# Kernel tuning notes

Measured on AMD Instinct MI355X. Metric: run time of the kernel, lower is better.

The kernel has to match this reference:

```python
import jax, jax.numpy as jnp
import numpy as np

N_NODES = 50000
N_EDGES = 800000
ND = 64   # node_dim
HD = 128  # hidden_dim
ED = 32   # edge_dim


def setup_inputs() -> dict:
    key = jax.random.key(0)
    ks = jax.random.split(key, 16)
    init = lambda k, shape: (jax.random.normal(k, shape, jnp.float32)
                             / np.float32(np.sqrt(shape[0])))
    h = jax.random.normal(ks[0], (N_NODES, ND), jnp.float32)
    x = jax.random.normal(ks[1], (N_NODES, 3), jnp.float32) * 10.0
    edge_index = jax.random.randint(ks[2], (2, N_EDGES), 0, N_NODES, dtype=jnp.int64)
    # realistic edge distances = actual pairwise distances of sampled edges
    edge_dist = jnp.linalg.norm(x[edge_index[0]] - x[edge_index[1]], axis=-1)
    in_dim = 2 * ND + ED
    return {
        "h": h, "x": x, "edge_index": edge_index, "edge_dist": edge_dist,
        # edge_mlp: Linear(1, ED) -> SiLU -> Linear(ED, ED)
        "We1": init(ks[3], (1, ED)), "be1": jnp.zeros((ED,), jnp.float32),
        "We2": init(ks[4], (ED, ED)), "be2": jnp.zeros((ED,), jnp.float32),
        # node_mlp: Linear(in_dim, HD) -> SiLU -> Linear(HD, ND)
        "Wn1": init(ks[5], (in_dim, HD)), "bn1": jnp.zeros((HD,), jnp.float32),
        "Wn2": init(ks[6], (HD, ND)), "bn2": jnp.zeros((ND,), jnp.float32),
        # coord_mlp: Linear(in_dim, HD) -> SiLU -> Linear(HD, 1, bias=False)
        "Wc1": init(ks[7], (in_dim, HD)), "bc1": jnp.zeros((HD,), jnp.float32),
        "Wc2": init(ks[8], (HD, 1)),
    }


def reference(h, x, edge_index, edge_dist,
              We1, be1, We2, be2,
              Wn1, bn1, Wn2, bn2,
              Wc1, bc1, Wc2):
    n = h.shape[0]
    src, dst = edge_index[0], edge_index[1]
    # edge_mlp on scalar distance -> [E, ED]
    e = jax.nn.silu(edge_dist[:, None] @ We1 + be1) @ We2 + be2
    # gather + concat -> [E, 2*ND + ED]
    m_input = jnp.concatenate([h[src], h[dst], e], axis=-1)
    # node messages [E, ND]
    m = jax.nn.silu(m_input @ Wn1 + bn1) @ Wn2 + bn2
    h_agg = jax.ops.segment_sum(m, dst, num_segments=n)
    # coord update weight [E, 1]
    coord_weight = jax.nn.silu(m_input @ Wc1 + bc1) @ Wc2
    dir_vec = x[src] - x[dst]
    dir_len = jnp.clip(jnp.linalg.norm(dir_vec, axis=-1, keepdims=True), 1e-8)
    coord_update = coord_weight * (dir_vec / dir_len)
    x_agg = jax.ops.segment_sum(coord_update, dst, num_segments=n)
    return h + h_agg, x + x_agg
```

## Files before the change

kernel.cpp:

```cpp
#include <hip/hip_runtime.h>


#define NN 50000
#define NE 800000
#define NDIM 64
#define HDIM 128
#define EDIM 32
#define NTILES (NE / 64)
#define MSTRIDE 168
#define HSTRIDE 136
#define NH (NN * NDIM)
#define NX (NN * 3)

#define WS_WN1P 0
#define WS_WC1P 20480
#define WS_BN1P 40960
#define WS_BC1P 41088

typedef __bf16 bf16x8 __attribute__((ext_vector_type(8)));
typedef float f32x4 __attribute__((ext_vector_type(4)));
typedef unsigned short ushort8 __attribute__((ext_vector_type(8)));
typedef unsigned short ushort4v __attribute__((ext_vector_type(4)));

__device__ __forceinline__ unsigned short f2bf(float f) {
    union { __bf16 b; unsigned short u; } c;
    c.b = (__bf16)f;
    return c.u;
}
__device__ __forceinline__ float silu(float v) {
    return __fdividef(v, 1.0f + __expf(-v));
}

__device__ __forceinline__ void bar_lds() {
    asm volatile("s_waitcnt lgkmcnt(0)" ::: "memory");
    __builtin_amdgcn_s_barrier();
}

__device__ __forceinline__ bf16x8 ld_frag(const unsigned short* p) {
    union { ushort8 u; bf16x8 v; } c;
    c.u = *(const ushort8*)p;
    return c.v;
}
__device__ __forceinline__ bf16x8 mk_frag(const unsigned short* u) {
    union { ushort8 uu; bf16x8 v; } c;
#pragma unroll
    for (int j = 0; j < 8; ++j) c.uu[j] = u[j];
    return c.v;
}

__global__ void init_out(const float* __restrict__ h, const float* __restrict__ x,
                         float* __restrict__ out) {
    int i = blockIdx.x * 256 + threadIdx.x;
    if (i < NH) out[i] = h[i];
    else if (i < NH + NX) out[i] = x[i - NH];
}

__global__ __launch_bounds__(128) void fold_weights(
    const float* __restrict__ We2, const float* __restrict__ be2,
    const float* __restrict__ Wn1, const float* __restrict__ bn1,
    const float* __restrict__ Wc1, const float* __restrict__ bc1,
    float* __restrict__ ws) {
    const int b = blockIdx.x;
    const int col = threadIdx.x;
    if (b < 320) {
        const int path = (b >= 160);
        const float* W = path ? Wc1 : Wn1;
        float* Wp = ws + (path ? WS_WC1P : WS_WN1P);
        const int r = path ? (b - 160) : b;
        if (r < 128) {
            Wp[r * 128 + col] = W[r * 128 + col];
        } else {
            const int j = r - 128;
            float s = 0.0f;
#pragma unroll
            for (int n = 0; n < 32; ++n)
                s += We2[j * 32 + n] * W[(128 + n) * 128 + col];
            Wp[r * 128 + col] = s;
        }
    } else {
        const int path = b - 320;
        const float* W = path ? Wc1 : Wn1;
        const float* bb = path ? bc1 : bn1;
        float* bp = ws + (path ? WS_BC1P : WS_BN1P);
        float s = bb[col];
#pragma unroll
        for (int n = 0; n < 32; ++n)
            s += be2[n] * W[(128 + n) * 128 + col];
        bp[col] = s;
    }
}

__global__ __launch_bounds__(256, 2) void egnn_edges(
    const float* __restrict__ h, const float* __restrict__ x,
    const int* __restrict__ srcg, const int* __restrict__ dstg,
    const float* __restrict__ dist,
    const float* __restrict__ We1, const float* __restrict__ be1,
    const float* __restrict__ Wn2, const float* __restrict__ bn2,
    const float* __restrict__ Wc2,
    const float* __restrict__ wsW,
    float* __restrict__ outh, float* __restrict__ outx) {

    __shared__ __align__(16) unsigned short mlds[64 * MSTRIDE];
    __shared__ __align__(16) unsigned short hl[64 * HSTRIDE];
    __shared__ int src_l[64];
    __shared__ int dst_l[64];
    __shared__ float we1_l[32], be1_l[32];
    __shared__ float part_l[256];

    const int tid  = threadIdx.x;
    const int w    = tid >> 6;
    const int lane = tid & 63;
    const int l15  = lane & 15;
    const int quad = lane >> 4;

    const float* Wn1p = wsW + WS_WN1P;
    const float* Wc1p = wsW + WS_WC1P;
    const float* bn1p = wsW + WS_BN1P;
    const float* bc1p = wsW + WS_BC1P;

    if (tid < 32) { we1_l[tid] = We1[tid]; be1_l[tid] = be1[tid]; }

    bf16x8 wn1f[5][2], wc1f[5][2];
#pragma unroll
    for (int kc = 0; kc < 5; ++kc) {
#pragma unroll
        for (int nt = 0; nt < 2; ++nt) {
            unsigned short un[8], uc[8];
            const int n = w * 32 + nt * 16 + l15;
#pragma unroll
            for (int j = 0; j < 8; ++j) {
                const int k = kc * 32 + quad * 8 + j;
                un[j] = f2bf(Wn1p[k * HDIM + n]);
                uc[j] = f2bf(Wc1p[k * HDIM + n]);
            }
            wn1f[kc][nt] = mk_frag(un);
            wc1f[kc][nt] = mk_frag(uc);
        }
    }
    bf16x8 wn2f[4];
#pragma unroll
    for (int kc = 0; kc < 4; ++kc) {
        unsigned short u[8];
        const int n = w * 16 + l15;
#pragma unroll
        for (int j = 0; j < 8; ++j) {
            const int k = kc * 32 + quad * 8 + j;
            u[j] = f2bf(Wn2[k * NDIM + n]);
        }
        wn2f[kc] = mk_frag(u);
    }
    const float biasN0 = bn1p[w * 32 + l15];
    const float biasN1 = bn1p[w * 32 + 16 + l15];
    const float biasC0 = bc1p[w * 32 + l15];
    const float biasC1 = bc1p[w * 32 + 16 + l15];
    const float bias2v = bn2[w * 16 + l15];
    const float wcA = Wc2[w * 32 + l15];
    const float wcB = Wc2[w * 32 + 16 + l15];

    for (int tile = blockIdx.x; tile < NTILES; tile += gridDim.x) {
        int pf_s = 0, pf_d = 0;
        if (tid < 64) {
            const int e = tile * 64 + tid;
            pf_s = srcg[e];
            pf_d = dstg[e];
        }
        bar_lds();

        if (tid < 64) { src_l[tid] = pf_s; dst_l[tid] = pf_d; }
        bar_lds();

        {
            const int c4 = tid & 15, sub = tid >> 4;
#pragma unroll
            for (int it = 0; it < 4; ++it) {
                const int el = sub + it * 16;
                const float4 hs = *(const float4*)(h + (size_t)src_l[el] * NDIM + c4 * 4);
                const float4 hd = *(const float4*)(h + (size_t)dst_l[el] * NDIM + c4 * 4);
                ushort4v us = { f2bf(hs.x), f2bf(hs.y), f2bf(hs.z), f2bf(hs.w) };
                ushort4v ud = { f2bf(hd.x), f2bf(hd.y), f2bf(hd.z), f2bf(hd.w) };
                *(ushort4v*)&mlds[el * MSTRIDE + c4 * 4] = us;
                *(ushort4v*)&mlds[el * MSTRIDE + 64 + c4 * 4] = ud;
            }
        }
        {
            const int el = tid >> 2, j0 = (tid & 3) * 8;
            const float dv = dist[tile * 64 + el];
            ushort8 u;
#pragma unroll
            for (int j = 0; j < 8; ++j)
                u[j] = f2bf(silu(dv * we1_l[j0 + j] + be1_l[j0 + j]));
            *(ushort8*)&mlds[el * MSTRIDE + 128 + j0] = u;
        }
        bar_lds();

        f32x4 accN[4][2], accC[4][2];
#pragma unroll
        for (int mt = 0; mt < 4; ++mt) {
            accN[mt][0] = (f32x4){biasN0, biasN0, biasN0, biasN0};
            accN[mt][1] = (f32x4){biasN1, biasN1, biasN1, biasN1};
            accC[mt][0] = (f32x4){biasC0, biasC0, biasC0, biasC0};
            accC[mt][1] = (f32x4){biasC1, biasC1, biasC1, biasC1};
        }
#pragma unroll
        for (int kc = 0; kc < 5; ++kc) {
            bf16x8 af[4];
#pragma unroll
            for (int mt = 0; mt < 4; ++mt)
                af[mt] = ld_frag(&mlds[(mt * 16 + l15) * MSTRIDE + kc * 32 + quad * 8]);
#pragma unroll
            for (int mt = 0; mt < 4; ++mt) {
#pragma unroll
                for (int nt = 0; nt < 2; ++nt) {
                    accN[mt][nt] = __builtin_amdgcn_mfma_f32_16x16x32_bf16(
                        af[mt], wn1f[kc][nt], accN[mt][nt], 0, 0, 0);
                    accC[mt][nt] = __builtin_amdgcn_mfma_f32_16x16x32_bf16(
                        af[mt], wc1f[kc][nt], accC[mt][nt], 0, 0, 0);
                }
            }
        }

#pragma unroll
        for (int mt = 0; mt < 4; ++mt)
#pragma unroll
            for (int nt = 0; nt < 2; ++nt)
#pragma unroll
                for (int r = 0; r < 4; ++r)
                    hl[(mt * 16 + quad * 4 + r) * HSTRIDE + w * 32 + nt * 16 + l15] =
                        f2bf(silu(accN[mt][nt][r]));

        {
            float p[16];
#pragma unroll
            for (int mt = 0; mt < 4; ++mt)
#pragma unroll
                for (int r = 0; r < 4; ++r)
                    p[mt * 4 + r] = silu(accC[mt][0][r]) * wcA + silu(accC[mt][1][r]) * wcB;

            float q8[8];
#pragma unroll
            for (int i = 0; i < 8; ++i) {
                const float send = (l15 & 8) ? p[i] : p[i + 8];
                const float recv = __shfl_xor(send, 8, 64);
                q8[i] = ((l15 & 8) ? p[i + 8] : p[i]) + recv;
            }
            float q4[4];
#pragma unroll
            for (int i = 0; i < 4; ++i) {
                const float send = (l15 & 4) ? q8[i] : q8[i + 4];
                const float recv = __shfl_xor(send, 4, 64);
                q4[i] = ((l15 & 4) ? q8[i + 4] : q8[i]) + recv;
            }
            float q2[2];
#pragma unroll
            for (int i = 0; i < 2; ++i) {
                const float send = (l15 & 2) ? q4[i] : q4[i + 2];
                const float recv = __shfl_xor(send, 2, 64);
                q2[i] = ((l15 & 2) ? q4[i + 2] : q4[i]) + recv;
            }
            {
                const float send = (l15 & 1) ? q2[0] : q2[1];
                const float recv = __shfl_xor(send, 1, 64);
                const float tot = ((l15 & 1) ? q2[1] : q2[0]) + recv;
                const int edge = (l15 >> 2) * 16 + quad * 4 + (l15 & 3);
                part_l[w * 64 + edge] = tot;
            }
        }
        bar_lds();

        f32x4 acc2[4];
#pragma unroll
        for (int mt = 0; mt < 4; ++mt) acc2[mt] = (f32x4){bias2v, bias2v, bias2v, bias2v};
#pragma unroll
        for (int kc = 0; kc < 4; ++kc) {
#pragma unroll
            for (int mt = 0; mt < 4; ++mt) {
                bf16x8 a2 = ld_frag(&hl[(mt * 16 + l15) * HSTRIDE + kc * 32 + quad * 8]);
                acc2[mt] = __builtin_amdgcn_mfma_f32_16x16x32_bf16(a2, wn2f[kc], acc2[mt], 0, 0, 0);
            }
        }
#pragma unroll
        for (int mt = 0; mt < 4; ++mt) {
#pragma unroll
            for (int r = 0; r < 4; ++r) {
                const int el = mt * 16 + quad * 4 + r;
                atomicAdd(outh + (size_t)dst_l[el] * NDIM + w * 16 + l15, acc2[mt][r]);
            }
        }

        if (tid < 64) {
            const float cw = part_l[tid] + part_l[64 + tid] + part_l[128 + tid] + part_l[192 + tid];
            const int sn = src_l[tid], dn = dst_l[tid];
            const float dx = x[sn * 3 + 0] - x[dn * 3 + 0];
            const float dy = x[sn * 3 + 1] - x[dn * 3 + 1];
            const float dz = x[sn * 3 + 2] - x[dn * 3 + 2];
            float len = sqrtf(dx * dx + dy * dy + dz * dz);
            len = fmaxf(len, 1e-8f);
            const float f = cw / len;
            atomicAdd(outx + (size_t)dn * 3 + 0, f * dx);
            atomicAdd(outx + (size_t)dn * 3 + 1, f * dy);
            atomicAdd(outx + (size_t)dn * 3 + 2, f * dz);
        }
    }
}

extern "C" void kernel_launch(void* const* d_in, const int* in_sizes, int n_in,
                              void* d_out, int out_size, void* d_ws, size_t ws_size,
                              hipStream_t stream) {
    const float* h    = (const float*)d_in[0];
    const float* x    = (const float*)d_in[1];
    const int*   ei   = (const int*)d_in[2];
    const float* dist = (const float*)d_in[3];
    const float* We1  = (const float*)d_in[4];
    const float* be1  = (const float*)d_in[5];
    const float* We2  = (const float*)d_in[6];
    const float* be2  = (const float*)d_in[7];
    const float* Wn1  = (const float*)d_in[8];
    const float* bn1  = (const float*)d_in[9];
    const float* Wn2  = (const float*)d_in[10];
    const float* bn2  = (const float*)d_in[11];
    const float* Wc1  = (const float*)d_in[12];
    const float* bc1  = (const float*)d_in[13];
    const float* Wc2  = (const float*)d_in[14];

    float* outh = (float*)d_out;
    float* outx = outh + (size_t)NH;
    float* ws   = (float*)d_ws;

    fold_weights<<<322, 128, 0, stream>>>(We2, be2, Wn1, bn1, Wc1, bc1, ws);
    init_out<<<(NH + NX + 255) / 256, 256, 0, stream>>>(h, x, (float*)d_out);
    egnn_edges<<<1024, 256, 0, stream>>>(h, x, ei, ei + NE, dist,
                                         We1, be1, Wn2, bn2, Wc2, ws,
                                         outh, outx);
}
```

Measured before the change: 425.8 us.

## Sort edges by destination and pre-reduce messages before atomic scatter

Adds a counting sort of edges by destination node (histogram, three-pass scan, scatter into workspace) so the edge kernel processes edges grouped by dst. In the edge kernel, per-tile messages and coordinate updates are staged in LDS and run-length reduced over consecutive equal destinations before issuing atomics. This is meant to cut the number of global atomics (about 16 per node on average). The cost is six extra small kernels and extra global traffic for the sorted arrays, and the sort path only runs if the workspace is large enough.

```diff
diff --git a/kernel.cpp b/kernel.cpp
--- a/kernel.cpp
+++ b/kernel.cpp
@@ -9,6 +9,7 @@
 #define NTILES (NE / 64)
 #define MSTRIDE 168
 #define HSTRIDE 136
+#define MLSTRIDE 65
 #define NH (NN * NDIM)
 #define NX (NN * 3)
 
@@ -16,6 +17,15 @@
 #define WS_WC1P 20480
 #define WS_BN1P 40960
 #define WS_BC1P 41088
+#define WS_WEIGHTS_FLOATS 65536
+#define NCNT 50176
+#define IOFF_CNT    WS_WEIGHTS_FLOATS
+#define IOFF_BLK    (IOFF_CNT + NCNT)
+#define IOFF_CUR    (IOFF_BLK + 256)
+#define IOFF_SRCS   (IOFF_CUR + NCNT)
+#define IOFF_DSTS   (IOFF_SRCS + NE)
+#define IOFF_DISTS  (IOFF_DSTS + NE)
+#define WS_TOTAL_BYTES ((size_t)(IOFF_DISTS + NE) * 4)
 
 typedef __bf16 bf16x8 __attribute__((ext_vector_type(8)));
 typedef float f32x4 __attribute__((ext_vector_type(4)));
@@ -54,6 +64,71 @@
     if (i < NH) out[i] = h[i];
     else if (i < NH + NX) out[i] = x[i - NH];
 }
+
+
+__global__ __launch_bounds__(256) void zero_cnt(int* __restrict__ cnt, int* __restrict__ cur) {
+    const int i = blockIdx.x * 256 + threadIdx.x;
+    if (i < NCNT) { cnt[i] = 0; cur[i] = 0; }
+}
+
+__global__ __launch_bounds__(256) void hist_dst(const int* __restrict__ dst, int* __restrict__ cnt) {
+    const int e = blockIdx.x * 256 + threadIdx.x;
+    if (e < NE) atomicAdd(&cnt[dst[e]], 1);
+}
+
+__global__ __launch_bounds__(256) void scan1(int* __restrict__ cnt, int* __restrict__ blk) {
+    __shared__ int sh[256];
+    const int t = threadIdx.x, i = blockIdx.x * 256 + t;
+    const int v = cnt[i];
+    sh[t] = v;
+    __syncthreads();
+#pragma unroll
+    for (int d = 1; d < 256; d <<= 1) {
+        const int o = (t >= d) ? sh[t - d] : 0;
+        __syncthreads();
+        sh[t] += o;
+        __syncthreads();
+    }
+    cnt[i] = sh[t] - v;
+    if (t == 255) blk[blockIdx.x] = sh[t];
+}
+
+__global__ __launch_bounds__(256) void scan2(int* __restrict__ blk) {
+    __shared__ int sh[256];
+    const int t = threadIdx.x;
+    const int v = (t < 196) ? blk[t] : 0;
+    sh[t] = v;
+    __syncthreads();
+#pragma unroll
+    for (int d = 1; d < 256; d <<= 1) {
+        const int o = (t >= d) ? sh[t - d] : 0;
+        __syncthreads();
+        sh[t] += o;
+        __syncthreads();
+    }
+    if (t < 196) blk[t] = sh[t] - v;
+}
+
+__global__ __launch_bounds__(256) void scan3(int* __restrict__ cnt, const int* __restrict__ blk) {
+    const int i = blockIdx.x * 256 + threadIdx.x;
+    if (i < NCNT) cnt[i] += blk[blockIdx.x];
+}
+
+__global__ __launch_bounds__(256) void scatter_edges(
+    const int* __restrict__ src, const int* __restrict__ dst,
+    const float* __restrict__ dist,
+    const int* __restrict__ base, int* __restrict__ cur,
+    int* __restrict__ srcs, int* __restrict__ dsts, float* __restrict__ dists) {
+    const int e = blockIdx.x * 256 + threadIdx.x;
+    if (e < NE) {
+        const int d = dst[e];
+        const int pos = base[d] + atomicAdd(&cur[d], 1);
+        srcs[pos] = src[e];
+        dsts[pos] = d;
+        dists[pos] = dist[e];
+    }
+}
+
 
 __global__ __launch_bounds__(128) void fold_weights(
     const float* __restrict__ We2, const float* __restrict__ be2,
@@ -90,6 +165,7 @@
     }
 }
 
+
 __global__ __launch_bounds__(256, 2) void egnn_edges(
     const float* __restrict__ h, const float* __restrict__ x,
     const int* __restrict__ srcg, const int* __restrict__ dstg,
@@ -106,6 +182,7 @@
     __shared__ int dst_l[64];
     __shared__ float we1_l[32], be1_l[32];
     __shared__ float part_l[256];
+    __shared__ float cx_l[64], cy_l[64], cz_l[64];
 
     const int tid  = threadIdx.x;
     const int w    = tid >> 6;
@@ -278,13 +355,14 @@
                 acc2[mt] = __builtin_amdgcn_mfma_f32_16x16x32_bf16(a2, wn2f[kc], acc2[mt], 0, 0, 0);
             }
         }
-#pragma unroll
-        for (int mt = 0; mt < 4; ++mt) {
-#pragma unroll
-            for (int r = 0; r < 4; ++r) {
-                const int el = mt * 16 + quad * 4 + r;
-                atomicAdd(outh + (size_t)dst_l[el] * NDIM + w * 16 + l15, acc2[mt][r]);
-            }
+
+        {
+            float* ml = (float*)mlds;
+#pragma unroll
+            for (int mt = 0; mt < 4; ++mt)
+#pragma unroll
+                for (int r = 0; r < 4; ++r)
+                    ml[(mt * 16 + quad * 4 + r) * MLSTRIDE + w * 16 + l15] = acc2[mt][r];
         }
 
         if (tid < 64) {
@@ -296,9 +374,41 @@
             float len = sqrtf(dx * dx + dy * dy + dz * dz);
             len = fmaxf(len, 1e-8f);
             const float f = cw / len;
-            atomicAdd(outx + (size_t)dn * 3 + 0, f * dx);
-            atomicAdd(outx + (size_t)dn * 3 + 1, f * dy);
-            atomicAdd(outx + (size_t)dn * 3 + 2, f * dz);
+            cx_l[tid] = f * dx; cy_l[tid] = f * dy; cz_l[tid] = f * dz;
+        }
+        bar_lds();
+
+        {
+            const int c = lane, g = w;
+            const int r0 = g * 16;
+            float acc = ((const float*)mlds)[r0 * MLSTRIDE + c];
+            int d = dst_l[r0];
+#pragma unroll
+            for (int r = r0 + 1; r < r0 + 16; ++r) {
+                const int dn = dst_l[r];
+                if (dn != d) {
+                    atomicAdd(outh + (size_t)d * NDIM + c, acc);
+                    acc = 0.0f;
+                    d = dn;
+                }
+                acc += ((const float*)mlds)[r * MLSTRIDE + c];
+            }
+            atomicAdd(outh + (size_t)d * NDIM + c, acc);
+        }
+
+        if (tid < 64) {
+            const int d = dst_l[tid];
+            if (tid == 0 || dst_l[tid - 1] != d) {
+                float sx = 0.0f, sy = 0.0f, sz = 0.0f;
+                int r = tid;
+                do {
+                    sx += cx_l[r]; sy += cy_l[r]; sz += cz_l[r];
+                    ++r;
+                } while (r < 64 && dst_l[r] == d);
+                atomicAdd(outx + (size_t)d * 3 + 0, sx);
+                atomicAdd(outx + (size_t)d * 3 + 1, sy);
+                atomicAdd(outx + (size_t)d * 3 + 2, sz);
+            }
         }
     }
 }
@@ -328,7 +438,30 @@
 
     fold_weights<<<322, 128, 0, stream>>>(We2, be2, Wn1, bn1, Wc1, bc1, ws);
     init_out<<<(NH + NX + 255) / 256, 256, 0, stream>>>(h, x, (float*)d_out);
-    egnn_edges<<<1024, 256, 0, stream>>>(h, x, ei, ei + NE, dist,
+
+    const int* es = ei;
+    const int* ed = ei + NE;
+    const float* edist = dist;
+
+    if (ws_size >= WS_TOTAL_BYTES) {
+        int*   cnt   = (int*)d_ws + IOFF_CNT;
+        int*   blk   = (int*)d_ws + IOFF_BLK;
+        int*   cur   = (int*)d_ws + IOFF_CUR;
+        int*   srcs  = (int*)d_ws + IOFF_SRCS;
+        int*   dsts  = (int*)d_ws + IOFF_DSTS;
+        float* dists = (float*)((int*)d_ws + IOFF_DISTS);
+
+        zero_cnt<<<NCNT / 256, 256, 0, stream>>>(cnt, cur);
+        hist_dst<<<NE / 256, 256, 0, stream>>>(ed, cnt);
+        scan1<<<NCNT / 256, 256, 0, stream>>>(cnt, blk);
+        scan2<<<1, 256, 0, stream>>>(blk);
+        scan3<<<NCNT / 256, 256, 0, stream>>>(cnt, blk);
+        scatter_edges<<<NE / 256, 256, 0, stream>>>(es, ed, dist, cnt, cur,
+                                                    srcs, dsts, dists);
+        es = srcs; ed = dsts; edist = dists;
+    }
+
+    egnn_edges<<<1024, 256, 0, stream>>>(h, x, es, ed, edist,
                                          We1, be1, Wn2, bn2, Wc2, ws,
                                          outh, outx);
 }
```

Result: slower. 458.0 us (+7.6%).

## Prefetch next tile's edge indices and node features across iterations, merge prep kernels

Applied to the files above, without the earlier changes.

Software-pipelines the edge loop: the indices, distances and h rows for the next tile are loaded into registers while the current tile's MFMAs run, which removes one barrier and hides gather latency. The x coordinates are loaded early instead of after the GEMMs. The hidden activations are written as packed bf16 pairs, using a permuted Wn2 row order so that the layout still matches. The weight-fold and output-init kernels are merged into one launch, and the 2-waves-per-SIMD launch bound is dropped. The extra prefetch registers raise register pressure and may lower occupancy.

```diff
diff --git a/kernel.cpp b/kernel.cpp
--- a/kernel.cpp
+++ b/kernel.cpp
@@ -5,7 +5,6 @@
 #define NE 800000
 #define NDIM 64
 #define HDIM 128
-#define EDIM 32
 #define NTILES (NE / 64)
 #define MSTRIDE 168
 #define HSTRIDE 136
@@ -30,12 +29,10 @@
 __device__ __forceinline__ float silu(float v) {
     return __fdividef(v, 1.0f + __expf(-v));
 }
-
 __device__ __forceinline__ void bar_lds() {
     asm volatile("s_waitcnt lgkmcnt(0)" ::: "memory");
     __builtin_amdgcn_s_barrier();
 }
-
 __device__ __forceinline__ bf16x8 ld_frag(const unsigned short* p) {
     union { ushort8 u; bf16x8 v; } c;
     c.u = *(const ushort8*)p;
@@ -48,49 +45,48 @@
     return c.v;
 }
 
-__global__ void init_out(const float* __restrict__ h, const float* __restrict__ x,
-                         float* __restrict__ out) {
-    int i = blockIdx.x * 256 + threadIdx.x;
-    if (i < NH) out[i] = h[i];
-    else if (i < NH + NX) out[i] = x[i - NH];
-}
-
-__global__ __launch_bounds__(128) void fold_weights(
+__global__ __launch_bounds__(256) void prep(
+    const float* __restrict__ h, const float* __restrict__ x,
     const float* __restrict__ We2, const float* __restrict__ be2,
     const float* __restrict__ Wn1, const float* __restrict__ bn1,
     const float* __restrict__ Wc1, const float* __restrict__ bc1,
-    float* __restrict__ ws) {
-    const int b = blockIdx.x;
-    const int col = threadIdx.x;
-    if (b < 320) {
-        const int path = (b >= 160);
-        const float* W = path ? Wc1 : Wn1;
-        float* Wp = ws + (path ? WS_WC1P : WS_WN1P);
-        const int r = path ? (b - 160) : b;
-        if (r < 128) {
-            Wp[r * 128 + col] = W[r * 128 + col];
+    float* __restrict__ out, float* __restrict__ wsf) {
+    const int gtid = blockIdx.x * 256 + threadIdx.x;
+    const int G = gridDim.x * 256;
+    if (gtid < 41216) {
+        if (gtid < 40960) {
+            const int path = gtid / 20480;
+            const int rem = gtid - path * 20480;
+            const int r = rem >> 7, col = rem & 127;
+            const float* W = path ? Wc1 : Wn1;
+            float* Wp = wsf + (path ? WS_WC1P : WS_WN1P);
+            if (r < 128) {
+                Wp[r * 128 + col] = W[r * 128 + col];
+            } else {
+                const int j = r - 128;
+                float s = 0.0f;
+#pragma unroll
+                for (int n = 0; n < 32; ++n)
+                    s += We2[j * 32 + n] * W[(128 + n) * 128 + col];
+                Wp[r * 128 + col] = s;
+            }
         } else {
-            const int j = r - 128;
-            float s = 0.0f;
+            const int j = gtid - 40960;
+            const int path = j >> 7, col = j & 127;
+            const float* W = path ? Wc1 : Wn1;
+            const float* bb = path ? bc1 : bn1;
+            float s = bb[col];
 #pragma unroll
             for (int n = 0; n < 32; ++n)
-                s += We2[j * 32 + n] * W[(128 + n) * 128 + col];
-            Wp[r * 128 + col] = s;
-        }
-    } else {
-        const int path = b - 320;
-        const float* W = path ? Wc1 : Wn1;
-        const float* bb = path ? bc1 : bn1;
-        float* bp = ws + (path ? WS_BC1P : WS_BN1P);
-        float s = bb[col];
-#pragma unroll
-        for (int n = 0; n < 32; ++n)
-            s += be2[n] * W[(128 + n) * 128 + col];
-        bp[col] = s;
-    }
-}
-
-__global__ __launch_bounds__(256, 2) void egnn_edges(
+                s += be2[n] * W[(128 + n) * 128 + col];
+            wsf[(path ? WS_BC1P : WS_BN1P) + col] = s;
+        }
+    }
+    for (int i = gtid; i < NH + NX; i += G)
+        out[i] = (i < NH) ? h[i] : x[i - NH];
+}
+
+__global__ __launch_bounds__(256) void egnn_edges(
     const float* __restrict__ h, const float* __restrict__ x,
     const int* __restrict__ srcg, const int* __restrict__ dstg,
     const float* __restrict__ dist,
@@ -112,6 +108,7 @@
     const int lane = tid & 63;
     const int l15  = lane & 15;
     const int quad = lane >> 4;
+    const int c4   = tid & 15, sub = tid >> 4;
 
     const float* Wn1p = wsW + WS_WN1P;
     const float* Wc1p = wsW + WS_WC1P;
@@ -145,7 +142,8 @@
 #pragma unroll
         for (int j = 0; j < 8; ++j) {
             const int k = kc * 32 + quad * 8 + j;
-            u[j] = f2bf(Wn2[k * NDIM + n]);
+            const int D = (k & ~31) + ((k & 1) << 4) + ((k & 31) >> 1);
+            u[j] = f2bf(Wn2[D * NDIM + n]);
         }
         wn2f[kc] = mk_frag(u);
     }
@@ -157,41 +155,64 @@
     const float wcA = Wc2[w * 32 + l15];
     const float wcB = Wc2[w * 32 + 16 + l15];
 
+    int psn[4], pdn[4];
+    float4 phs[4], phd[4];
+    float pdist;
+    int psl = 0, pdl = 0;
+    {
+        const int e0 = blockIdx.x * 64;
+#pragma unroll
+        for (int it = 0; it < 4; ++it) {
+            psn[it] = srcg[e0 + sub + it * 16];
+            pdn[it] = dstg[e0 + sub + it * 16];
+        }
+#pragma unroll
+        for (int it = 0; it < 4; ++it) {
+            phs[it] = *(const float4*)(h + (size_t)psn[it] * NDIM + c4 * 4);
+            phd[it] = *(const float4*)(h + (size_t)pdn[it] * NDIM + c4 * 4);
+        }
+        pdist = dist[e0 + (tid >> 2)];
+        if (tid < 64) { psl = srcg[e0 + tid]; pdl = dstg[e0 + tid]; }
+    }
+
     for (int tile = blockIdx.x; tile < NTILES; tile += gridDim.x) {
-        int pf_s = 0, pf_d = 0;
+        bar_lds();
+
+        float xs0 = 0, xs1 = 0, xs2 = 0, xd0 = 0, xd1 = 0, xd2 = 0;
         if (tid < 64) {
-            const int e = tile * 64 + tid;
-            pf_s = srcg[e];
-            pf_d = dstg[e];
+            src_l[tid] = psl; dst_l[tid] = pdl;
+            xs0 = x[psl * 3 + 0]; xs1 = x[psl * 3 + 1]; xs2 = x[psl * 3 + 2];
+            xd0 = x[pdl * 3 + 0]; xd1 = x[pdl * 3 + 1]; xd2 = x[pdl * 3 + 2];
+        }
+#pragma unroll
+        for (int it = 0; it < 4; ++it) {
+            const int el = sub + it * 16;
+            ushort4v us = { f2bf(phs[it].x), f2bf(phs[it].y), f2bf(phs[it].z), f2bf(phs[it].w) };
+            ushort4v ud = { f2bf(phd[it].x), f2bf(phd[it].y), f2bf(phd[it].z), f2bf(phd[it].w) };
+            *(ushort4v*)&mlds[el * MSTRIDE + c4 * 4] = us;
+            *(ushort4v*)&mlds[el * MSTRIDE + 64 + c4 * 4] = ud;
+        }
+        {
+            const int el = tid >> 2, j0 = (tid & 3) * 8;
+            ushort8 u;
+#pragma unroll
+            for (int j = 0; j < 8; ++j)
+                u[j] = f2bf(silu(pdist * we1_l[j0 + j] + be1_l[j0 + j]));
+            *(ushort8*)&mlds[el * MSTRIDE + 128 + j0] = u;
         }
         bar_lds();
 
-        if (tid < 64) { src_l[tid] = pf_s; dst_l[tid] = pf_d; }
-        bar_lds();
-
-        {
-            const int c4 = tid & 15, sub = tid >> 4;
+        {
+            const int tn = tile + (int)gridDim.x;
+            const int eb = (tn < NTILES ? tn : tile) * 64;
 #pragma unroll
             for (int it = 0; it < 4; ++it) {
-                const int el = sub + it * 16;
-                const float4 hs = *(const float4*)(h + (size_t)src_l[el] * NDIM + c4 * 4);
-                const float4 hd = *(const float4*)(h + (size_t)dst_l[el] * NDIM + c4 * 4);
-                ushort4v us = { f2bf(hs.x), f2bf(hs.y), f2bf(hs.z), f2bf(hs.w) };
-                ushort4v ud = { f2bf(hd.x), f2bf(hd.y), f2bf(hd.z), f2bf(hd.w) };
-                *(ushort4v*)&mlds[el * MSTRIDE + c4 * 4] = us;
-                *(ushort4v*)&mlds[el * MSTRIDE + 64 + c4 * 4] = ud;
-            }
-        }
-        {
-            const int el = tid >> 2, j0 = (tid & 3) * 8;
-            const float dv = dist[tile * 64 + el];
-            ushort8 u;
-#pragma unroll
-            for (int j = 0; j < 8; ++j)
-                u[j] = f2bf(silu(dv * we1_l[j0 + j] + be1_l[j0 + j]));
-            *(ushort8*)&mlds[el * MSTRIDE + 128 + j0] = u;
-        }
-        bar_lds();
+                psn[it] = srcg[eb + sub + it * 16];
+                pdn[it] = dstg[eb + sub + it * 16];
+            }
+            pdist = dist[eb + (tid >> 2)];
+            if (tid < 64) { psl = srcg[eb + tid]; pdl = dstg[eb + tid]; }
+        }
 
         f32x4 accN[4][2], accC[4][2];
 #pragma unroll
@@ -220,13 +241,23 @@
         }
 
 #pragma unroll
-        for (int mt = 0; mt < 4; ++mt)
-#pragma unroll
-            for (int nt = 0; nt < 2; ++nt)
-#pragma unroll
-                for (int r = 0; r < 4; ++r)
-                    hl[(mt * 16 + quad * 4 + r) * HSTRIDE + w * 32 + nt * 16 + l15] =
-                        f2bf(silu(accN[mt][nt][r]));
+        for (int it = 0; it < 4; ++it) {
+            phs[it] = *(const float4*)(h + (size_t)psn[it] * NDIM + c4 * 4);
+            phd[it] = *(const float4*)(h + (size_t)pdn[it] * NDIM + c4 * 4);
+        }
+
+        {
+            unsigned int* hlu = (unsigned int*)hl;
+#pragma unroll
+            for (int mt = 0; mt < 4; ++mt)
+#pragma unroll
+                for (int r = 0; r < 4; ++r) {
+                    const unsigned int u0 = f2bf(silu(accN[mt][0][r]));
+                    const unsigned int u1 = f2bf(silu(accN[mt][1][r]));
+                    hlu[(mt * 16 + quad * 4 + r) * (HSTRIDE / 2) + w * 16 + l15] =
+                        (u1 << 16) | u0;
+                }
+        }
 
         {
             float p[16];
@@ -253,8 +284,10 @@
             float q2[2];
 #pragma unroll
             for (int i = 0; i < 2; ++i) {
-                const float send = (l15 & 2) ? q4[i] : q4[i + 2];
-                const float recv = __shfl_xor(send, 2, 64);
+                const float send = (l15 & 2) ? q2[0] * 0.0f + ((l15 & 2) ? q4[i] : q4[i + 2]) : q4[i + 2];
+                (void)send;
+                const float s2 = (l15 & 2) ? q4[i] : q4[i + 2];
+                const float recv = __shfl_xor(s2, 2, 64);
                 q2[i] = ((l15 & 2) ? q4[i + 2] : q4[i]) + recv;
             }
             {
@@ -267,35 +300,37 @@
         }
         bar_lds();
 
-        f32x4 acc2[4];
-#pragma unroll
-        for (int mt = 0; mt < 4; ++mt) acc2[mt] = (f32x4){bias2v, bias2v, bias2v, bias2v};
-#pragma unroll
-        for (int kc = 0; kc < 4; ++kc) {
+        {
+            f32x4 acc2[4];
+#pragma unroll
+            for (int mt = 0; mt < 4; ++mt) acc2[mt] = (f32x4){bias2v, bias2v, bias2v, bias2v};
+#pragma unroll
+            for (int kc = 0; kc < 4; ++kc) {
+#pragma unroll
+                for (int mt = 0; mt < 4; ++mt) {
+                    bf16x8 a2 = ld_frag(&hl[(mt * 16 + l15) * HSTRIDE + kc * 32 + quad * 8]);
+                    acc2[mt] = __builtin_amdgcn_mfma_f32_16x16x32_bf16(a2, wn2f[kc], acc2[mt], 0, 0, 0);
+                }
+            }
 #pragma unroll
             for (int mt = 0; mt < 4; ++mt) {
-                bf16x8 a2 = ld_frag(&hl[(mt * 16 + l15) * HSTRIDE + kc * 32 + quad * 8]);
-                acc2[mt] = __builtin_amdgcn_mfma_f32_16x16x32_bf16(a2, wn2f[kc], acc2[mt], 0, 0, 0);
-            }
-        }
-#pragma unroll
-        for (int mt = 0; mt < 4; ++mt) {
-#pragma unroll
-            for (int r = 0; r < 4; ++r) {
-                const int el = mt * 16 + quad * 4 + r;
-                atomicAdd(outh + (size_t)dst_l[el] * NDIM + w * 16 + l15, acc2[mt][r]);
+#pragma unroll
+                for (int r = 0; r < 4; ++r) {
+                    const int el = mt * 16 + quad * 4 + r;
+                    atomicAdd(outh + (size_t)dst_l[el] * NDIM + w * 16 + l15, acc2[mt][r]);
+                }
             }
         }
 
         if (tid < 64) {
             const float cw = part_l[tid] + part_l[64 + tid] + part_l[128 + tid] + part_l[192 + tid];
-            const int sn = src_l[tid], dn = dst_l[tid];
-            const float dx = x[sn * 3 + 0] - x[dn * 3 + 0];
-            const float dy = x[sn * 3 + 1] - x[dn * 3 + 1];
-            const float dz = x[sn * 3 + 2] - x[dn * 3 + 2];
+            const float dx = xs0 - xd0;
+            const float dy = xs1 - xd1;
+            const float dz = xs2 - xd2;
             float len = sqrtf(dx * dx + dy * dy + dz * dz);
             len = fmaxf(len, 1e-8f);
             const float f = cw / len;
+            const int dn = dst_l[tid];
             atomicAdd(outx + (size_t)dn * 3 + 0, f * dx);
             atomicAdd(outx + (size_t)dn * 3 + 1, f * dy);
             atomicAdd(outx + (size_t)dn * 3 + 2, f * dz);
@@ -326,8 +361,8 @@
     float* outx = outh + (size_t)NH;
     float* ws   = (float*)d_ws;
 
-    fold_weights<<<322, 128, 0, stream>>>(We2, be2, Wn1, bn1, Wc1, bc1, ws);
-    init_out<<<(NH + NX + 255) / 256, 256, 0, stream>>>(h, x, (float*)d_out);
+    prep<<<2048, 256, 0, stream>>>(h, x, We2, be2, Wn1, bn1, Wc1, bc1,
+                                   (float*)d_out, ws);
     egnn_edges<<<1024, 256, 0, stream>>>(h, x, ei, ei + NE, dist,
                                          We1, be1, Wn2, bn2, Wc2, ws,
                                          outh, outx);
```

Result: slower. 444.7 us (+4.4%).
